# Kernel tuning notes

Measured on AMD Instinct MI355X. Metric: run time of the kernel, lower is better.

## Reference

```python
import jax, jax.numpy as jnp
import numpy as np

B, N, D, H = 1, 4096, 1024, 16
E = D // H  # head_dim = 64


def setup_inputs() -> dict:
    key = jax.random.key(0)
    ks = jax.random.split(key, 5)
    s = 0.02
    return {
        "query": jax.random.normal(ks[0], (B, N, D), dtype=jnp.float32),
        "Wq": jax.random.normal(ks[1], (D, D), dtype=jnp.float32) * s,
        "Wk": jax.random.normal(ks[2], (D, D), dtype=jnp.float32) * s,
        "Wv": jax.random.normal(ks[3], (D, D), dtype=jnp.float32) * s,
        "Wo": jax.random.normal(ks[4], (D, D), dtype=jnp.float32) * s,
        "bo": jnp.zeros((D,), dtype=jnp.float32),
    }


def reference(query, Wq, Wk, Wv, Wo, bo):
    # self-attention: key = value = query
    # nn.Linear: y = x @ W.T  (weights stored as [out, in])
    q = query @ Wq.T  # [b, n, d]
    k = query @ Wk.T
    v = query @ Wv.T
    # 'b n (h e) -> b h n e'
    q = q.reshape(B, N, H, E).transpose(0, 2, 1, 3)
    k = k.reshape(B, N, H, E).transpose(0, 2, 1, 3)
    v = v.reshape(B, N, H, E).transpose(0, 2, 1, 3)
    scale = 1.0 / jnp.sqrt(jnp.asarray(E, dtype=q.dtype))
    attn = jnp.einsum('bhne,bhme->bhnm', q, k) * scale  # [b, h, n, n]
    attn = jax.nn.softmax(attn, axis=-1)
    out = jnp.einsum('bhnm,bhme->bhne', attn, v)  # [b, h, n, e]
    # 'b h n e -> b n (h e)'
    out = out.transpose(0, 2, 1, 3).reshape(B, N, D)
    out = out @ Wo.T + bo
    return out
```

## Files before the change

### kernel.cpp

```cpp
#include <hip/hip_runtime.h>


typedef __attribute__((ext_vector_type(8))) __bf16 bf16x8;
typedef __attribute__((ext_vector_type(4))) float f32x4;
typedef __attribute__((ext_vector_type(16))) float f32x16;
typedef __attribute__((ext_vector_type(4))) unsigned short us4;
typedef __attribute__((ext_vector_type(4))) unsigned int u32x4;
typedef __attribute__((ext_vector_type(2))) unsigned int u32x2;

#define DEV __device__ __forceinline__

#define QSCALE 0.1803368801111204f

DEV unsigned short f2bf(float x) {
  union { float f; unsigned u; } c; c.f = x;
  unsigned u = c.u;
  u += 0x7FFFu + ((u >> 16) & 1u);
  return (unsigned short)(u >> 16);
}

DEV float expq(float x) {
#if __has_builtin(__builtin_amdgcn_exp2f)
  return __builtin_amdgcn_exp2f(x);
#else
  float r;
  asm("v_exp_f32 %0, %1" : "=v"(r) : "v"(x));
  return r;
#endif
}

DEV unsigned cvtpk_bf16(float lo, float hi) {
  unsigned r;
  asm("v_cvt_pk_bf16_f32 %0, %1, %2" : "=v"(r) : "v"(lo), "v"(hi));
  return r;
}

DEV void plswap_u(unsigned& a, unsigned& b) {
#if __has_builtin(__builtin_amdgcn_permlane32_swap)
  u32x2 r = __builtin_amdgcn_permlane32_swap(a, b, false, false);
  a = r.x; b = r.y;
#else
  asm("v_permlane32_swap_b32 %0, %1" : "+v"(a), "+v"(b));
#endif
}

DEV void plswap_f(float& a, float& b) {
  unsigned ua = __float_as_uint(a), ub = __float_as_uint(b);
  plswap_u(ua, ub);
  a = __uint_as_float(ua); b = __uint_as_float(ub);
}

DEV void gload16(const void* g, void* lds) {
  __builtin_amdgcn_global_load_lds(
      (const __attribute__((address_space(1))) unsigned int*)g,
      (__attribute__((address_space(3))) unsigned int*)lds, 16, 0, 0);
}

__global__ void cast_bf16_kernel(const float* __restrict__ in,
                                 unsigned short* __restrict__ out, int n4) {
  int i = blockIdx.x * 256 + threadIdx.x;
  if (i >= n4) return;
  float4 v = reinterpret_cast<const float4*>(in)[i];
  us4 o;
  o.x = f2bf(v.x); o.y = f2bf(v.y); o.z = f2bf(v.z); o.w = f2bf(v.w);
  reinterpret_cast<us4*>(out)[i] = o;
}

__global__ void cast4_bf16_kernel(const float* __restrict__ a,
                                  const float* __restrict__ b,
                                  const float* __restrict__ c,
                                  const float* __restrict__ d,
                                  unsigned short* __restrict__ out, int n4) {
  const int y = blockIdx.y;
  const float* src = y == 0 ? a : (y == 1 ? b : (y == 2 ? c : d));
  int i = blockIdx.x * 256 + threadIdx.x;
  if (i >= n4) return;
  float4 v = reinterpret_cast<const float4*>(src)[i];
  us4 o;
  o.x = f2bf(v.x); o.y = f2bf(v.y); o.z = f2bf(v.z); o.w = f2bf(v.w);
  reinterpret_cast<us4*>(out + (size_t)y * n4 * 4)[i] = o;
}

__global__ void repack_v(const unsigned short* __restrict__ V,
                         unsigned short* __restrict__ Vp) {
  __shared__ unsigned short tile[64][65];
  const int t = threadIdx.x;
  const int bc = blockIdx.x * 64;
  const int br = blockIdx.y * 64;
#pragma unroll
  for (int i = 0; i < 16; ++i) {
    int idx = i * 256 + t;
    int r = idx >> 6, c = idx & 63;
    tile[r][c] = V[(size_t)(br + r) * 1024 + bc + c];
  }
  __syncthreads();
  const int obase = ((bc >> 6) * 64 + (br >> 6)) * 4096;
#pragma unroll
  for (int i = 0; i < 16; ++i) {
    int id = i * 256 + t;
    int f = id >> 9, rem = id & 511, e = rem >> 3, kv8 = rem & 7;
    Vp[obase + id] = tile[f * 8 + kv8][e];
  }
}

__global__ __launch_bounds__(256)
void gemm_qkv(const unsigned short* __restrict__ A,
              const unsigned short* __restrict__ B,
              unsigned short* __restrict__ Qo,
              unsigned short* __restrict__ Ko,
              unsigned short* __restrict__ Vo) {
  constexpr int K = 1024, BK = 64;
  __shared__ unsigned short As[128 * BK];
  __shared__ unsigned short Bs[128 * BK];
  const int t = threadIdx.x;
  const int w = t >> 6, l = t & 63;
  const int brow = blockIdx.x * 128;
  const int bcol = blockIdx.y * 128;
  const int wr = w >> 1, wc = w & 1;
  const int lr = l >> 3;
  const int lc = ((l & 7) ^ lr) * 8;
  const int fr = l & 15;
  const int fcb = (l >> 4) * 16;
  const int swz = (l & 7) << 4;

  f32x4 acc[4][4] = {};
  const char* Asb = (const char*)As;
  const char* Bsb = (const char*)Bs;

  for (int k0 = 0; k0 < K; k0 += BK) {
#pragma unroll
    for (int i = 0; i < 4; ++i) {
      const int r = w * 32 + i * 8;
      gload16(A + (size_t)(brow + r + lr) * K + k0 + lc, (void*)(As + r * BK));
      gload16(B + (size_t)(bcol + r + lr) * K + k0 + lc, (void*)(Bs + r * BK));
    }
    __syncthreads();
#pragma unroll
    for (int kk = 0; kk < 2; ++kk) {
      bf16x8 af[4], bfr[4];
#pragma unroll
      for (int m = 0; m < 4; ++m)
        af[m] = *(const bf16x8*)(Asb + (wr * 64 + m * 16 + fr) * 128 +
                                 ((kk * 64 + fcb) ^ swz));
#pragma unroll
      for (int n = 0; n < 4; ++n)
        bfr[n] = *(const bf16x8*)(Bsb + (wc * 64 + n * 16 + fr) * 128 +
                                  ((kk * 64 + fcb) ^ swz));
#pragma unroll
      for (int m = 0; m < 4; ++m)
#pragma unroll
        for (int n = 0; n < 4; ++n)
          acc[m][n] = __builtin_amdgcn_mfma_f32_16x16x32_bf16(
              af[m], bfr[n], acc[m][n], 0, 0, 0);
    }
    __syncthreads();
  }

  const int seg = blockIdx.y >> 3;
  const int orow = brow + wr * 64 + (l >> 4) * 4;
  const int ocol = (blockIdx.y & 7) * 128 + wc * 64 + fr;
  if (seg == 1) {
#pragma unroll
    for (int n = 0; n < 4; ++n) {
      const int col = ocol + n * 16;
      const int bn = (col >> 6) * 262144 + ((col & 63) >> 3) * 512 + (col & 7);
#pragma unroll
      for (int m = 0; m < 4; ++m)
#pragma unroll
        for (int j = 0; j < 4; ++j) {
          const int row = orow + m * 16 + j;
          Ko[bn + (row >> 6) * 4096 + (row & 63) * 8] = f2bf(acc[m][n][j]);
        }
    }
  } else {
    unsigned short* dst = seg == 0 ? Qo : Vo;
    const float sc = seg == 0 ? QSCALE : 1.0f;
#pragma unroll
    for (int m = 0; m < 4; ++m)
#pragma unroll
      for (int n = 0; n < 4; ++n)
#pragma unroll
        for (int j = 0; j < 4; ++j)
          dst[(size_t)(orow + m * 16 + j) * 1024 + (ocol + n * 16)] =
              f2bf(acc[m][n][j] * sc);
  }
}

__global__ __launch_bounds__(256)
void gemm_out64(const unsigned short* __restrict__ A,
                const unsigned short* __restrict__ B,
                float* __restrict__ C, const float* __restrict__ bias) {
  constexpr int N = 1024, K = 1024, BK = 64;
  __shared__ unsigned short As[64 * BK];
  __shared__ unsigned short Bs[128 * BK];
  const int t = threadIdx.x;
  const int w = t >> 6, l = t & 63;
  const int brow = blockIdx.x * 64;
  const int bcol = blockIdx.y * 128;
  const int wr = w >> 1, wc = w & 1;
  const int lr = l >> 3;
  const int lc = ((l & 7) ^ lr) * 8;
  const int fr = l & 15;
  const int fcb = (l >> 4) * 16;
  const int swz = (l & 7) << 4;

  f32x4 acc[2][4] = {};
  const char* Asb = (const char*)As;
  const char* Bsb = (const char*)Bs;

  for (int k0 = 0; k0 < K; k0 += BK) {
#pragma unroll
    for (int i = 0; i < 2; ++i) {
      const int r = w * 16 + i * 8;
      gload16(A + (size_t)(brow + r + lr) * K + k0 + lc, (void*)(As + r * BK));
    }
#pragma unroll
    for (int i = 0; i < 4; ++i) {
      const int r = w * 32 + i * 8;
      gload16(B + (size_t)(bcol + r + lr) * K + k0 + lc, (void*)(Bs + r * BK));
    }
    __syncthreads();
#pragma unroll
    for (int kk = 0; kk < 2; ++kk) {
      bf16x8 af[2], bfr[4];
#pragma unroll
      for (int m = 0; m < 2; ++m)
        af[m] = *(const bf16x8*)(Asb + (wr * 32 + m * 16 + fr) * 128 +
                                 ((kk * 64 + fcb) ^ swz));
#pragma unroll
      for (int n = 0; n < 4; ++n)
        bfr[n] = *(const bf16x8*)(Bsb + (wc * 64 + n * 16 + fr) * 128 +
                                  ((kk * 64 + fcb) ^ swz));
#pragma unroll
      for (int m = 0; m < 2; ++m)
#pragma unroll
        for (int n = 0; n < 4; ++n)
          acc[m][n] = __builtin_amdgcn_mfma_f32_16x16x32_bf16(
              af[m], bfr[n], acc[m][n], 0, 0, 0);
    }
    __syncthreads();
  }

  const int orow = brow + wr * 32 + (l >> 4) * 4;
  const int ocol = bcol + wc * 64 + fr;
#pragma unroll
  for (int m = 0; m < 2; ++m)
#pragma unroll
    for (int n = 0; n < 4; ++n)
#pragma unroll
      for (int j = 0; j < 4; ++j)
        C[(size_t)(orow + m * 16 + j) * N + (ocol + n * 16)] =
            acc[m][n][j] + bias[ocol + n * 16];
}

__global__ __launch_bounds__(512, 4)
void attn_v8(const unsigned short* __restrict__ Q,
             const unsigned short* __restrict__ Kp,
             const unsigned short* __restrict__ Vp,
             unsigned short* __restrict__ AO) {
  constexpr int N = 4096, D = 1024, NT = N / 64;
  __shared__ unsigned long long LDSA[65536 / 8];
  char* LDS = (char*)LDSA;
  const int t = threadIdx.x, w = t >> 6, l = t & 63;
  const int g = w >> 2, wg = w & 3;
  const int flat = blockIdx.x;
  const int c = flat & 7, ii = flat >> 3;
  const int h = c * 2 + (ii >> 5);
  const int qt = ii & 31;
  const int q0 = qt * 128 + wg * 32;
  const int ln = l & 31, hi = l >> 5;
  const int lr = l >> 3;
  const int ko = hi * 1024 + ln * 16;

  char* kb0 = LDS + (g * 2 + 0) * 8192;
  char* kb1 = LDS + (g * 2 + 1) * 8192;
  char* vb0 = LDS + 32768 + (g * 2 + 0) * 8192;
  char* vb1 = LDS + 32768 + (g * 2 + 1) * 8192;

  bf16x8 qf[4];
  {
    const unsigned short* qp = Q + (size_t)(q0 + ln) * D + h * 64 + hi * 8;
#pragma unroll
    for (int ks = 0; ks < 4; ++ks) qf[ks] = *(const bf16x8*)(qp + ks * 16);
  }

  f32x16 oacc0 = {}, oacc1 = {};
  float lsum = 0.f;

  const char* Kp8 = (const char*)Kp;
  const char* Vp8 = (const char*)Vp;

  auto stage = [&](char* kd, char* vd, int kvt) {
    const char* Kt = Kp8 + (size_t)(h * 64 + kvt) * 8192;
    const char* Vt = Vp8 + (size_t)(h * 64 + kvt) * 8192;
#pragma unroll
    for (int s = 0; s < 2; ++s) {
      const int off = (wg * 2 + s) * 1024;
      gload16(Kt + off + l * 16, (void*)(kd + off));
      gload16(Vt + off + l * 16, (void*)(vd + off));
    }
  };

  stage(kb0, vb0, g);
  __syncthreads();

  for (int i = 0; i < NT / 2; ++i) {
    const char* ksb = (i & 1) ? kb1 : kb0;
    const char* vsb = (i & 1) ? vb1 : vb0;
    if (i + 1 < NT / 2)
      stage((i & 1) ? kb0 : kb1, (i & 1) ? vb0 : vb1, 2 * (i + 1) + g);

    f32x16 sa = {}, sb = {};
    __builtin_amdgcn_s_setprio(1);
#pragma unroll
    for (int ks = 0; ks < 4; ++ks) {
      bf16x8 kf0 = *(const bf16x8*)(ksb + ks * 2048 + ko);
      bf16x8 kf1 = *(const bf16x8*)(ksb + ks * 2048 + 512 + ko);
      sa = __builtin_amdgcn_mfma_f32_32x32x16_bf16(kf0, qf[ks], sa, 0, 0, 0);
      sb = __builtin_amdgcn_mfma_f32_32x32x16_bf16(kf1, qf[ks], sb, 0, 0, 0);
    }
    __builtin_amdgcn_s_setprio(0);

#pragma unroll
    for (int r = 0; r < 16; ++r) { sa[r] = expq(sa[r]); sb[r] = expq(sb[r]); }
    {
      float red[16];
#pragma unroll
      for (int r = 0; r < 16; ++r) red[r] = sa[r] + sb[r];
#pragma unroll
      for (int s = 8; s >= 1; s >>= 1)
#pragma unroll
        for (int r = 0; r < s; ++r) red[r] += red[r + s];
      lsum += red[0];
    }

    unsigned pw[4][4];
#pragma unroll
    for (int kvs = 0; kvs < 4; ++kvs) {
      const f32x16& S = (kvs < 2) ? sa : sb;
      const int rb = (kvs & 1) * 8;
      unsigned A0 = cvtpk_bf16(S[rb + 0], S[rb + 1]);
      unsigned B0 = cvtpk_bf16(S[rb + 4], S[rb + 5]);
      unsigned A1 = cvtpk_bf16(S[rb + 2], S[rb + 3]);
      unsigned B1 = cvtpk_bf16(S[rb + 6], S[rb + 7]);
      plswap_u(A0, B0);
      plswap_u(A1, B1);
      pw[kvs][0] = A0; pw[kvs][1] = A1; pw[kvs][2] = B0; pw[kvs][3] = B1;
    }

    __builtin_amdgcn_s_setprio(1);
#pragma unroll
    for (int kvs = 0; kvs < 4; ++kvs) {
      u32x4 pv = {pw[kvs][0], pw[kvs][1], pw[kvs][2], pw[kvs][3]};
      bf16x8 pf = __builtin_bit_cast(bf16x8, pv);
      bf16x8 vf0 = *(const bf16x8*)(vsb + kvs * 2048 + ko);
      bf16x8 vf1 = *(const bf16x8*)(vsb + kvs * 2048 + 512 + ko);
      oacc0 = __builtin_amdgcn_mfma_f32_32x32x16_bf16(vf0, pf, oacc0, 0, 0, 0);
      oacc1 = __builtin_amdgcn_mfma_f32_32x32x16_bf16(vf1, pf, oacc1, 0, 0, 0);
    }
    __builtin_amdgcn_s_setprio(0);

    __syncthreads();
  }

  float* cb = (float*)LDS;
  float* cl = (float*)(LDS + 32768);
  if (g == 1) {
    float* p = cb + (wg * 64 + l) * 32;
#pragma unroll
    for (int r = 0; r < 16; ++r) { p[r] = oacc0[r]; p[16 + r] = oacc1[r]; }
    cl[wg * 64 + l] = lsum;
  }
  __syncthreads();
  if (g == 0) {
    float* p = cb + (wg * 64 + l) * 32;
#pragma unroll
    for (int r = 0; r < 16; ++r) { oacc0[r] += p[r]; oacc1[r] += p[16 + r]; }
    lsum += cl[wg * 64 + l];
    float sa2 = lsum, sb2 = lsum;
    plswap_f(sa2, sb2);
    const float inv = 1.0f / (sa2 + sb2);

    char* Osc = LDS + 34816 + wg * 4096;
#pragma unroll
    for (int es = 0; es < 2; ++es)
#pragma unroll
      for (int gg = 0; gg < 4; ++gg)
#pragma unroll
        for (int c2 = 0; c2 < 2; ++c2) {
          const f32x16& oa = es == 0 ? oacc0 : oacc1;
          unsigned pk = cvtpk_bf16(oa[gg * 4 + c2 * 2] * inv,
                                   oa[gg * 4 + c2 * 2 + 1] * inv);
          const int col = es * 64 + gg * 16 + hi * 8 + c2 * 4;
          *(unsigned*)(Osc + ln * 128 + (col ^ ((ln & 7) << 4))) = pk;
        }
#pragma unroll
    for (int p2 = 0; p2 < 4; ++p2) {
      const int q = p2 * 8 + lr;
      bf16x8 ov = *(const bf16x8*)(Osc + q * 128 + (((l & 7) ^ lr) << 4));
      *(bf16x8*)(AO + (size_t)(q0 + q) * D + h * 64 + (l & 7) * 8) = ov;
    }
  }
}

extern "C" void kernel_launch(void* const* d_in, const int* in_sizes, int n_in,
                              void* d_out, int out_size, void* d_ws, size_t ws_size,
                              hipStream_t stream) {
  const float* query = (const float*)d_in[0];
  const float* Wq    = (const float*)d_in[1];
  const float* Wk    = (const float*)d_in[2];
  const float* Wv    = (const float*)d_in[3];
  const float* Wo    = (const float*)d_in[4];
  const float* bo    = (const float*)d_in[5];
  float* out = (float*)d_out;

  char* ws = (char*)d_ws;
  const size_t MB = 1024 * 1024;
  unsigned short* Wqkv_b = (unsigned short*)(ws + 0 * MB);
  unsigned short* Wo_b   = (unsigned short*)(ws + 6 * MB);
  unsigned short* Xb     = (unsigned short*)(ws + 8 * MB);
  unsigned short* Qb     = (unsigned short*)(ws + 16 * MB);
  unsigned short* Kb     = (unsigned short*)(ws + 24 * MB);
  unsigned short* Vb     = (unsigned short*)(ws + 32 * MB);
  unsigned short* Vtb    = (unsigned short*)(ws + 40 * MB);
  unsigned short* AOb    = (unsigned short*)(ws + 32 * MB);

  {
    int n4 = (4096 * 1024) / 4;
    cast_bf16_kernel<<<dim3((n4 + 255) / 256), dim3(256), 0, stream>>>(query, Xb, n4);
    n4 = (1024 * 1024) / 4;
    cast4_bf16_kernel<<<dim3((n4 + 255) / 256, 4), dim3(256), 0, stream>>>(
        Wq, Wk, Wv, Wo, Wqkv_b, n4);
  }

  gemm_qkv<<<dim3(32, 24), dim3(256), 0, stream>>>(Xb, Wqkv_b, Qb, Kb, Vb);

  repack_v<<<dim3(16, 64), dim3(256), 0, stream>>>(Vb, Vtb);

  attn_v8<<<dim3(512), dim3(512), 0, stream>>>(Qb, Kb, Vtb, AOb);

  gemm_out64<<<dim3(64, 8), dim3(256), 0, stream>>>(AOb, Wo_b, out, bo);
}
```

Baseline: 151.5 us.

## Fuse casts, write V in packed layout from QKV GEMM, MFMA row sums

Merges the activation and weight bf16 casts into a single launch. The QKV GEMM now writes V directly in the packed tile layout, so the separate repack_v kernel and its extra pass over V are gone. In the attention kernel, softmax row sums are now computed with an extra MFMA against a ones vector instead of a VALU reduction plus a permlane swap. The KV staging is also restructured so each wave group loads interleaved tiles with simpler addressing. The cost is one extra MFMA per kv step and scattered 2-byte stores for V in the GEMM epilogue.

```diff
diff --git a/kernel.cpp b/kernel.cpp
--- a/kernel.cpp
+++ b/kernel.cpp
@@ -44,63 +44,34 @@
 #endif
 }
 
-DEV void plswap_f(float& a, float& b) {
-  unsigned ua = __float_as_uint(a), ub = __float_as_uint(b);
-  plswap_u(ua, ub);
-  a = __uint_as_float(ua); b = __uint_as_float(ub);
-}
-
 DEV void gload16(const void* g, void* lds) {
   __builtin_amdgcn_global_load_lds(
       (const __attribute__((address_space(1))) unsigned int*)g,
       (__attribute__((address_space(3))) unsigned int*)lds, 16, 0, 0);
 }
 
-__global__ void cast_bf16_kernel(const float* __restrict__ in,
-                                 unsigned short* __restrict__ out, int n4) {
-  int i = blockIdx.x * 256 + threadIdx.x;
-  if (i >= n4) return;
-  float4 v = reinterpret_cast<const float4*>(in)[i];
-  us4 o;
-  o.x = f2bf(v.x); o.y = f2bf(v.y); o.z = f2bf(v.z); o.w = f2bf(v.w);
-  reinterpret_cast<us4*>(out)[i] = o;
-}
-
-__global__ void cast4_bf16_kernel(const float* __restrict__ a,
-                                  const float* __restrict__ b,
-                                  const float* __restrict__ c,
-                                  const float* __restrict__ d,
-                                  unsigned short* __restrict__ out, int n4) {
+__global__ void cast_all(const float* __restrict__ q,
+                         const float* __restrict__ wa,
+                         const float* __restrict__ wb,
+                         const float* __restrict__ wc,
+                         const float* __restrict__ wd,
+                         unsigned short* __restrict__ qo,
+                         unsigned short* __restrict__ wout) {
   const int y = blockIdx.y;
-  const float* src = y == 0 ? a : (y == 1 ? b : (y == 2 ? c : d));
-  int i = blockIdx.x * 256 + threadIdx.x;
-  if (i >= n4) return;
+  const int i = blockIdx.x * 256 + threadIdx.x;
+  const float* src;
+  unsigned short* dst;
+  if (y < 4) {
+    src = q + (size_t)y * 1048576;
+    dst = qo + (size_t)y * 1048576;
+  } else {
+    src = (y == 4) ? wa : (y == 5) ? wb : (y == 6) ? wc : wd;
+    dst = wout + (size_t)(y - 4) * 1048576;
+  }
   float4 v = reinterpret_cast<const float4*>(src)[i];
   us4 o;
   o.x = f2bf(v.x); o.y = f2bf(v.y); o.z = f2bf(v.z); o.w = f2bf(v.w);
-  reinterpret_cast<us4*>(out + (size_t)y * n4 * 4)[i] = o;
-}
-
-__global__ void repack_v(const unsigned short* __restrict__ V,
-                         unsigned short* __restrict__ Vp) {
-  __shared__ unsigned short tile[64][65];
-  const int t = threadIdx.x;
-  const int bc = blockIdx.x * 64;
-  const int br = blockIdx.y * 64;
-#pragma unroll
-  for (int i = 0; i < 16; ++i) {
-    int idx = i * 256 + t;
-    int r = idx >> 6, c = idx & 63;
-    tile[r][c] = V[(size_t)(br + r) * 1024 + bc + c];
-  }
-  __syncthreads();
-  const int obase = ((bc >> 6) * 64 + (br >> 6)) * 4096;
-#pragma unroll
-  for (int i = 0; i < 16; ++i) {
-    int id = i * 256 + t;
-    int f = id >> 9, rem = id & 511, e = rem >> 3, kv8 = rem & 7;
-    Vp[obase + id] = tile[f * 8 + kv8][e];
-  }
+  reinterpret_cast<us4*>(dst)[i] = o;
 }
 
 __global__ __launch_bounds__(256)
@@ -162,27 +133,39 @@
   if (seg == 1) {
 #pragma unroll
     for (int n = 0; n < 4; ++n) {
-      const int col = ocol + n * 16;
-      const int bn = (col >> 6) * 262144 + ((col & 63) >> 3) * 512 + (col & 7);
+      const int C = ocol + n * 16;
+      const int bn = (C >> 6) * 262144 + ((C & 63) >> 3) * 512 + (C & 7);
 #pragma unroll
       for (int m = 0; m < 4; ++m)
 #pragma unroll
         for (int j = 0; j < 4; ++j) {
-          const int row = orow + m * 16 + j;
-          Ko[bn + (row >> 6) * 4096 + (row & 63) * 8] = f2bf(acc[m][n][j]);
+          const int R = orow + m * 16 + j;
+          Ko[bn + (R >> 6) * 4096 + (R & 63) * 8] = f2bf(acc[m][n][j]);
         }
     }
+  } else if (seg == 2) {
+#pragma unroll
+    for (int n = 0; n < 4; ++n) {
+      const int C = ocol + n * 16;
+      const int bn = (C >> 6) * 262144 + (C & 63) * 8;
+#pragma unroll
+      for (int m = 0; m < 4; ++m)
+#pragma unroll
+        for (int j = 0; j < 4; ++j) {
+          const int R = orow + m * 16 + j;
+          Vo[bn + (R >> 6) * 4096 + ((R & 63) >> 3) * 512 + (R & 7)] =
+              f2bf(acc[m][n][j]);
+        }
+    }
   } else {
-    unsigned short* dst = seg == 0 ? Qo : Vo;
-    const float sc = seg == 0 ? QSCALE : 1.0f;
 #pragma unroll
     for (int m = 0; m < 4; ++m)
 #pragma unroll
       for (int n = 0; n < 4; ++n)
 #pragma unroll
         for (int j = 0; j < 4; ++j)
-          dst[(size_t)(orow + m * 16 + j) * 1024 + (ocol + n * 16)] =
-              f2bf(acc[m][n][j] * sc);
+          Qo[(size_t)(orow + m * 16 + j) * 1024 + (ocol + n * 16)] =
+              f2bf(acc[m][n][j] * QSCALE);
   }
 }
 
@@ -254,7 +237,7 @@
 }
 
 __global__ __launch_bounds__(512, 4)
-void attn_v8(const unsigned short* __restrict__ Q,
+void attn_v9(const unsigned short* __restrict__ Q,
              const unsigned short* __restrict__ Kp,
              const unsigned short* __restrict__ Vp,
              unsigned short* __restrict__ AO) {
@@ -283,32 +266,34 @@
 #pragma unroll
     for (int ks = 0; ks < 4; ++ks) qf[ks] = *(const bf16x8*)(qp + ks * 16);
   }
-
-  f32x16 oacc0 = {}, oacc1 = {};
-  float lsum = 0.f;
-
-  const char* Kp8 = (const char*)Kp;
-  const char* Vp8 = (const char*)Vp;
-
-  auto stage = [&](char* kd, char* vd, int kvt) {
-    const char* Kt = Kp8 + (size_t)(h * 64 + kvt) * 8192;
-    const char* Vt = Vp8 + (size_t)(h * 64 + kvt) * 8192;
-#pragma unroll
-    for (int s = 0; s < 2; ++s) {
-      const int off = (wg * 2 + s) * 1024;
-      gload16(Kt + off + l * 16, (void*)(kd + off));
-      gload16(Vt + off + l * 16, (void*)(vd + off));
-    }
+  bf16x8 onesf;
+  {
+    u32x4 ov = {0x3F803F80u, 0x3F803F80u, 0x3F803F80u, 0x3F803F80u};
+    onesf = __builtin_bit_cast(bf16x8, ov);
+  }
+
+  f32x16 oacc0 = {}, oacc1 = {}, dsum = {};
+
+  const int stoff = wg * 2048;
+  const char* Kg = (const char*)Kp + ((size_t)(h * 64 + g)) * 8192 + stoff + l * 16;
+  const char* Vg = (const char*)Vp + ((size_t)(h * 64 + g)) * 8192 + stoff + l * 16;
+
+  auto stage = [&](char* kd, char* vd, int it) {
+    const size_t o = (size_t)it * 16384;
+    gload16(Kg + o, kd + stoff);
+    gload16(Kg + o + 1024, kd + stoff + 1024);
+    gload16(Vg + o, vd + stoff);
+    gload16(Vg + o + 1024, vd + stoff + 1024);
   };
 
-  stage(kb0, vb0, g);
+  stage(kb0, vb0, 0);
   __syncthreads();
 
   for (int i = 0; i < NT / 2; ++i) {
     const char* ksb = (i & 1) ? kb1 : kb0;
     const char* vsb = (i & 1) ? vb1 : vb0;
     if (i + 1 < NT / 2)
-      stage((i & 1) ? kb0 : kb1, (i & 1) ? vb0 : vb1, 2 * (i + 1) + g);
+      stage((i & 1) ? kb0 : kb1, (i & 1) ? vb0 : vb1, i + 1);
 
     f32x16 sa = {}, sb = {};
     __builtin_amdgcn_s_setprio(1);
@@ -323,16 +308,6 @@
 
 #pragma unroll
     for (int r = 0; r < 16; ++r) { sa[r] = expq(sa[r]); sb[r] = expq(sb[r]); }
-    {
-      float red[16];
-#pragma unroll
-      for (int r = 0; r < 16; ++r) red[r] = sa[r] + sb[r];
-#pragma unroll
-      for (int s = 8; s >= 1; s >>= 1)
-#pragma unroll
-        for (int r = 0; r < s; ++r) red[r] += red[r + s];
-      lsum += red[0];
-    }
 
     unsigned pw[4][4];
 #pragma unroll
@@ -355,6 +330,7 @@
       bf16x8 pf = __builtin_bit_cast(bf16x8, pv);
       bf16x8 vf0 = *(const bf16x8*)(vsb + kvs * 2048 + ko);
       bf16x8 vf1 = *(const bf16x8*)(vsb + kvs * 2048 + 512 + ko);
+      dsum = __builtin_amdgcn_mfma_f32_32x32x16_bf16(onesf, pf, dsum, 0, 0, 0);
       oacc0 = __builtin_amdgcn_mfma_f32_32x32x16_bf16(vf0, pf, oacc0, 0, 0, 0);
       oacc1 = __builtin_amdgcn_mfma_f32_32x32x16_bf16(vf1, pf, oacc1, 0, 0, 0);
     }
@@ -369,17 +345,14 @@
     float* p = cb + (wg * 64 + l) * 32;
 #pragma unroll
     for (int r = 0; r < 16; ++r) { p[r] = oacc0[r]; p[16 + r] = oacc1[r]; }
-    cl[wg * 64 + l] = lsum;
+    cl[wg * 64 + l] = dsum[0];
   }
   __syncthreads();
   if (g == 0) {
     float* p = cb + (wg * 64 + l) * 32;
 #pragma unroll
     for (int r = 0; r < 16; ++r) { oacc0[r] += p[r]; oacc1[r] += p[16 + r]; }
-    lsum += cl[wg * 64 + l];
-    float sa2 = lsum, sb2 = lsum;
-    plswap_f(sa2, sb2);
-    const float inv = 1.0f / (sa2 + sb2);
+    const float inv = 1.0f / (dsum[0] + cl[wg * 64 + l]);
 
     char* Osc = LDS + 34816 + wg * 4096;
 #pragma unroll
@@ -421,23 +394,15 @@
   unsigned short* Xb     = (unsigned short*)(ws + 8 * MB);
   unsigned short* Qb     = (unsigned short*)(ws + 16 * MB);
   unsigned short* Kb     = (unsigned short*)(ws + 24 * MB);
-  unsigned short* Vb     = (unsigned short*)(ws + 32 * MB);
   unsigned short* Vtb    = (unsigned short*)(ws + 40 * MB);
   unsigned short* AOb    = (unsigned short*)(ws + 32 * MB);
 
-  {
-    int n4 = (4096 * 1024) / 4;
-    cast_bf16_kernel<<<dim3((n4 + 255) / 256), dim3(256), 0, stream>>>(query, Xb, n4);
-    n4 = (1024 * 1024) / 4;
-    cast4_bf16_kernel<<<dim3((n4 + 255) / 256, 4), dim3(256), 0, stream>>>(
-        Wq, Wk, Wv, Wo, Wqkv_b, n4);
-  }
-
-  gemm_qkv<<<dim3(32, 24), dim3(256), 0, stream>>>(Xb, Wqkv_b, Qb, Kb, Vb);
-
-  repack_v<<<dim3(16, 64), dim3(256), 0, stream>>>(Vb, Vtb);
-
-  attn_v8<<<dim3(512), dim3(512), 0, stream>>>(Qb, Kb, Vtb, AOb);
+  cast_all<<<dim3(1024, 8), dim3(256), 0, stream>>>(query, Wq, Wk, Wv, Wo,
+                                                    Xb, Wqkv_b);
+
+  gemm_qkv<<<dim3(32, 24), dim3(256), 0, stream>>>(Xb, Wqkv_b, Qb, Kb, Vtb);
+
+  attn_v9<<<dim3(512), dim3(512), 0, stream>>>(Qb, Kb, Vtb, AOb);
 
   gemm_out64<<<dim3(64, 8), dim3(256), 0, stream>>>(AOb, Wo_b, out, bo);
 }
```

New measurement: 148.1 us. 2.2% less time.
